# Optimization experiments

Measured on AMD Instinct MI355X. Metric: run time of the kernel, lower is better.

The kernel has to match this reference:

```python
import jax, jax.numpy as jnp
import numpy as np
from jax.scipy.linalg import expm

N, D, COND_DIM = 1152, 64, 1152
B, T = 16, 1024


def setup_inputs() -> dict:
    key = jax.random.key(0)
    k1, k2, k3, k4, k5 = jax.random.split(key, 5)
    x = jax.random.normal(k1, (B, T, N), dtype=jnp.float32)
    cond = jax.random.normal(k2, (B, COND_DIM), dtype=jnp.float32)
    # learned parameters
    P = jax.random.normal(k3, (N, D), dtype=jnp.float32)
    n_skew = D * (D - 1) // 2
    # nn.Linear default init: U(-1/sqrt(fan_in), 1/sqrt(fan_in))
    bound = 1.0 / np.sqrt(COND_DIM)
    W = jax.random.uniform(k4, (n_skew, COND_DIM), minval=-bound, maxval=bound, dtype=jnp.float32)
    b = jax.random.uniform(k5, (n_skew,), minval=-bound, maxval=bound, dtype=jnp.float32)
    return {"x": x, "cond": cond, "P": P, "W": W, "b": b}


def _rotation(cond, W, b):
    # SiLU -> Linear -> skew-symmetric A -> matrix exponential
    v = jax.nn.silu(cond) @ W.T + b  # (B, D*(D-1)//2)
    iu, ju = jnp.triu_indices(D, k=1)
    A = jnp.zeros((cond.shape[0], D, D), dtype=v.dtype)
    A = A.at[:, iu, ju].set(v).at[:, ju, iu].set(-v)
    return expm(A)  # batched over leading dim, (B, D, D)


def reference(x, cond, P, W, b):
    U, _ = jnp.linalg.qr(P)          # (N, D) orthonormal basis of subspace
    R = _rotation(cond, W, b)        # (B, D, D)
    z = jnp.einsum('btn,nd->btd', x, U)          # project into subspace
    z_rot = jnp.einsum('btd,bde->bte', z, R)     # rotate within subspace
    x_rot = x + jnp.einsum('btd,nd->btn', z_rot - z, U)  # (z_rot - z) @ U.T
    return x_rot
```

## Files before the change

### kernel.cpp

```cpp
#include <hip/hip_runtime.h>
#include <math.h>

#define NN 1152
#define DD 64
#define NSK 2016
#define NB 16
#define NROWS (NB*1024)
#define GPARTS 6
#define KPARTS 6
#define VNBLK 32
#define VBLKS (VNBLK*KPARTS)

typedef short bf16x8 __attribute__((ext_vector_type(8)));
typedef short bf16x4 __attribute__((ext_vector_type(4)));
typedef float f32x4  __attribute__((ext_vector_type(4)));

__device__ __forceinline__ short bfr(float f){
  unsigned u = __float_as_uint(f);
  u += 0x7fffu + ((u >> 16) & 1u);
  return (short)(u >> 16);
}

__global__ __launch_bounds__(256) void k_pre(const float* __restrict__ cond, const float* __restrict__ W,
                                             float* __restrict__ vpart,
                                             const float* __restrict__ P, float* __restrict__ Gpart){
  __shared__ float Ps[64*68];
  const int tid = threadIdx.x;
  if (blockIdx.x < VBLKS){
    const int nb = blockIdx.x / KPARTS;
    const int kp = blockIdx.x % KPARTS;
    const int lane = tid & 63, wid = tid >> 6;
    const int m = lane & 15, quad = lane >> 4;
    const int n0 = nb*64 + wid*16;
    if (n0 >= NSK) return;
    f32x4 acc = {0.f,0.f,0.f,0.f};
    const float* crow = &cond[m*NN + kp*192 + quad*8];
    const float* wrow = &W[(n0 + m)*NN + kp*192 + quad*8];
    #pragma unroll
    for (int c = 0; c < 6; ++c){
      const float4 ca = *(const float4*)(crow + c*32);
      const float4 cb = *(const float4*)(crow + c*32 + 4);
      const float4 wa = *(const float4*)(wrow + c*32);
      const float4 wb = *(const float4*)(wrow + c*32 + 4);
      bf16x8 a, b;
      const float cv[8] = {ca.x,ca.y,ca.z,ca.w,cb.x,cb.y,cb.z,cb.w};
      const float wv[8] = {wa.x,wa.y,wa.z,wa.w,wb.x,wb.y,wb.z,wb.w};
      #pragma unroll
      for (int j = 0; j < 8; ++j){
        const float xv = cv[j];
        a[j] = bfr(xv / (1.f + __expf(-xv)));
        b[j] = bfr(wv[j]);
      }
      acc = __builtin_amdgcn_mfma_f32_16x16x32_bf16(a, b, acc, 0, 0, 0);
    }
    #pragma unroll
    for (int r = 0; r < 4; ++r)
      vpart[(kp*16 + quad*4 + r)*NSK + n0 + m] = acc[r];
  } else {
    const int p = blockIdx.x - VBLKS;
    const int lr = tid >> 4, lc = (tid & 15) * 4;
    const int ti = tid >> 4, tj = tid & 15;
    float acc[4][4];
    #pragma unroll
    for (int i=0;i<4;++i){
      #pragma unroll
      for (int j=0;j<4;++j) acc[i][j]=0.f;
    }
    for (int ch = 0; ch < 3; ++ch){
      const int nn0 = p*192 + ch*64;
      __syncthreads();
      #pragma unroll
      for (int ii = 0; ii < 4; ++ii){
        const float4 pv = *(const float4*)&P[(nn0 + lr + 16*ii)*DD + lc];
        *(float4*)&Ps[(lr + 16*ii)*68 + lc] = pv;
      }
      __syncthreads();
      for (int r = 0; r < 64; ++r){
        const float4 a = *(const float4*)&Ps[r*68 + ti*4];
        const float4 b = *(const float4*)&Ps[r*68 + tj*4];
        const float av[4] = {a.x,a.y,a.z,a.w};
        const float bv[4] = {b.x,b.y,b.z,b.w};
        #pragma unroll
        for (int i=0;i<4;++i){
          #pragma unroll
          for (int j=0;j<4;++j) acc[i][j] = fmaf(av[i], bv[j], acc[i][j]);
        }
      }
    }
    float* g = &Gpart[p*DD*DD];
    #pragma unroll
    for (int i=0;i<4;++i){
      float4 ov = make_float4(acc[i][0], acc[i][1], acc[i][2], acc[i][3]);
      *(float4*)&g[(ti*4+i)*DD + tj*4] = ov;
    }
  }
}

__device__ void qr_wave(const float* __restrict__ Gpart, const float* __restrict__ P,
                        float* __restrict__ Rout){
  const int j = threadIdx.x;
  float Gc[DD], Wc[DD], Rc[DD];
  #pragma unroll
  for (int i = 0; i < DD; ++i){
    float g = 0.f;
    #pragma unroll
    for (int p = 0; p < GPARTS; ++p) g += Gpart[p*4096 + i*DD + j];
    Gc[i] = g;
    Wc[i] = P[i*DD + j];
  }
  #pragma unroll
  for (int k = 0; k < DD; ++k){
    const float gkk = __shfl(Gc[k], k);
    const float wkk = __shfl(Wc[k], k);
    const float beta = (wkk >= 0.f) ? -sqrtf(gkk) : sqrtf(gkk);
    const float wkj = Wc[k];
    const float dj  = Gc[k] - beta*wkj;
    const float cj  = dj / (beta*(beta - wkk));
    float rkj = wkj + dj/beta;
    if (j == k) rkj = beta;
    if (j <  k) rkj = 0.f;
    Rc[k] = rkj;
    #pragma unroll
    for (int i = k+1; i < DD; ++i){
      const float wik = __shfl(Wc[i], k);
      const float rki = __shfl(rkj, i);
      Wc[i] = fmaf(-cj,  wik, Wc[i]);
      Gc[i] = fmaf(-rki, rkj, Gc[i]);
    }
  }
  #pragma unroll
  for (int i = 0; i < DD; ++i) Rout[i*DD + j] = Rc[i];
}

__device__ __forceinline__ void mmul68(const float* __restrict__ A, const float* __restrict__ B,
                                       float* __restrict__ C, int tid){
  __syncthreads();
  const int w = tid >> 6, lane = tid & 63;
  const int r0 = (w & 3) * 16 + (lane >> 3) * 2;
  const int c0 = (w >> 2) * 32 + (lane & 7) * 4;
  float acc[2][4];
  #pragma unroll
  for (int i=0;i<2;++i){
    #pragma unroll
    for (int j=0;j<4;++j) acc[i][j]=0.f;
  }
  for (int kq = 0; kq < 16; ++kq){
    float4 b[4];
    #pragma unroll
    for (int kk=0;kk<4;++kk) b[kk] = *(const float4*)&B[(kq*4+kk)*68 + c0];
    const float4 a0 = *(const float4*)&A[(r0    )*68 + kq*4];
    const float4 a1 = *(const float4*)&A[(r0 + 1)*68 + kq*4];
    const float av0[4] = {a0.x,a0.y,a0.z,a0.w};
    const float av1[4] = {a1.x,a1.y,a1.z,a1.w};
    #pragma unroll
    for (int kk=0;kk<4;++kk){
      acc[0][0] = fmaf(av0[kk], b[kk].x, acc[0][0]);
      acc[0][1] = fmaf(av0[kk], b[kk].y, acc[0][1]);
      acc[0][2] = fmaf(av0[kk], b[kk].z, acc[0][2]);
      acc[0][3] = fmaf(av0[kk], b[kk].w, acc[0][3]);
      acc[1][0] = fmaf(av1[kk], b[kk].x, acc[1][0]);
      acc[1][1] = fmaf(av1[kk], b[kk].y, acc[1][1]);
      acc[1][2] = fmaf(av1[kk], b[kk].z, acc[1][2]);
      acc[1][3] = fmaf(av1[kk], b[kk].w, acc[1][3]);
    }
  }
  *(float4*)&C[(r0    )*68 + c0] = make_float4(acc[0][0],acc[0][1],acc[0][2],acc[0][3]);
  *(float4*)&C[(r0 + 1)*68 + c0] = make_float4(acc[1][0],acc[1][1],acc[1][2],acc[1][3]);
  __syncthreads();
}

__global__ __launch_bounds__(512,1) void k_setup(const float* __restrict__ Gpart, const float* __restrict__ P,
                                                 float* __restrict__ Rout,
                                                 const float* __restrict__ vpart, const float* __restrict__ bias,
                                                 float* __restrict__ Mg){
  __shared__ float Bs[64*68], B2[64*68], B3[64*68], Tb[64*68], Xb[64*68];
  __shared__ float red[512];
  __shared__ float scl_s;
  __shared__ int   ssh_s;
  const int tid = threadIdx.x;
  if (blockIdx.x == NB){
    if (tid >= 64) return;
    qr_wave(Gpart, P, Rout);
    return;
  }
  const int b = blockIdx.x;
  for (int idx = tid; idx < 64*64; idx += 512)
    Xb[(idx>>6)*68 + (idx&63)] = 0.f;
  __syncthreads();
  for (int idx = tid; idx < NSK; idx += 512){
    int i = (int)((127.0f - sqrtf(16129.0f - 8.0f*(float)idx)) * 0.5f);
    while (i*(127 - i)/2 > idx) --i;
    while ((i+1)*(127 - (i+1))/2 <= idx) ++i;
    const int jj = idx - i*(127 - i)/2 + i + 1;
    float val = bias[idx];
    #pragma unroll
    for (int p = 0; p < KPARTS; ++p) val += vpart[(p*16 + b)*NSK + idx];
    Xb[i*68 + jj] = val;
    Xb[jj*68 + i] = -val;
  }
  __syncthreads();
  {
    const int c = tid & 63, g = tid >> 6;
    float s = 0.f;
    for (int r = g*8; r < g*8 + 8; ++r) s += fabsf(Xb[r*68 + c]);
    red[g*64 + c] = s;
    __syncthreads();
    if (tid < 64){
      float cs = 0.f;
      #pragma unroll
      for (int g2 = 0; g2 < 8; ++g2) cs += red[g2*64 + tid];
      #pragma unroll
      for (int off = 32; off > 0; off >>= 1) cs = fmaxf(cs, __shfl_xor(cs, off));
      if (tid == 0){
        int s2 = 0; float scale = 1.f;
        float nrm = cs;
        while (nrm > 1.0f && s2 < 40){ nrm *= 0.5f; scale *= 0.5f; ++s2; }
        ssh_s = s2; scl_s = scale;
      }
    }
    __syncthreads();
  }
  const float scale = scl_s;
  const int   sq    = ssh_s;
  for (int idx = tid; idx < 64*64; idx += 512){
    const int i = idx>>6, jj = idx&63;
    Bs[i*68 + jj] = Xb[i*68 + jj] * scale;
  }
  mmul68(Bs, Bs, B2, tid);
  mmul68(B2, Bs, B3, tid);
  for (int idx = tid; idx < 64*64; idx += 512){
    const int i = idx>>6, jj = idx&63;
    const int o = i*68 + jj;
    Tb[o] = (i==jj ? (1.f/720.f) : 0.f) + Bs[o]*(1.f/5040.f) + B2[o]*(1.f/40320.f) + B3[o]*(1.f/362880.f);
  }
  mmul68(B3, Tb, Xb, tid);
  for (int idx = tid; idx < 64*64; idx += 512){
    const int i = idx>>6, jj = idx&63;
    const int o = i*68 + jj;
    Xb[o] += (i==jj ? (1.f/6.f) : 0.f) + Bs[o]*(1.f/24.f) + B2[o]*(1.f/120.f);
  }
  mmul68(B3, Xb, Tb, tid);
  for (int idx = tid; idx < 64*64; idx += 512){
    const int i = idx>>6, jj = idx&63;
    const int o = i*68 + jj;
    Tb[o] += (i==jj ? 1.f : 0.f) + Bs[o] + B2[o]*0.5f;
  }
  float* cur = Tb;
  float* oth = Xb;
  for (int r = 0; r < sq; ++r){
    mmul68(cur, cur, oth, tid);
    float* t = cur; cur = oth; oth = t;
  }
  for (int idx = tid; idx < 64*64; idx += 512){
    const int i = idx>>6, jj = idx&63;
    Mg[b*4096 + idx] = cur[i*68 + jj] - (i==jj ? 1.f : 0.f);
  }
}

__global__ __launch_bounds__(64) void k_solveU(const float* __restrict__ P, const float* __restrict__ Rg,
                                               short* __restrict__ Ubf, short* __restrict__ Utbf){
  __shared__ float Rs[DD*DD];
  __shared__ float Ps[DD*65];
  __shared__ float rd[DD];
  const int tid = threadIdx.x;
  const int n0 = blockIdx.x * DD;
  for (int r = 0; r < DD; ++r){
    Rs[r*DD + tid] = Rg[r*DD + tid];
    Ps[r*65 + tid] = P[(n0 + r)*DD + tid];
  }
  rd[tid] = 1.f / Rg[tid*DD + tid];
  __syncthreads();
  float u[DD];
  #pragma unroll
  for (int j = 0; j < DD; ++j){
    float s0 = Ps[tid*65 + j], s1 = 0.f;
    #pragma unroll
    for (int l = 0; l + 1 < j; l += 2){
      s0 = fmaf(-u[l],   Rs[l*DD + j],     s0);
      s1 = fmaf(-u[l+1], Rs[(l+1)*DD + j], s1);
    }
    if (j & 1) s0 = fmaf(-u[j-1], Rs[(j-1)*DD + j], s0);
    u[j] = (s0 + s1) * rd[j];
  }
  #pragma unroll
  for (int d = 0; d < DD; ++d)
    Utbf[d*NN + n0 + tid] = bfr(u[d]);
  #pragma unroll
  for (int j8 = 0; j8 < 8; ++j8){
    bf16x8 pk;
    #pragma unroll
    for (int jj = 0; jj < 8; ++jj) pk[jj] = bfr(u[j8*8 + jj]);
    *(bf16x8*)&Ubf[(n0 + tid)*DD + j8*8] = pk;
  }
}

__global__ __launch_bounds__(512,1) void k_zw(const float* __restrict__ x, const short* __restrict__ Utbf,
                                              const float* __restrict__ Mg, short* __restrict__ wg){
  __shared__ float zs[64*68];
  __shared__ float Ms[64*68];
  const int tid  = threadIdx.x;
  const int lane = tid & 63, wid = tid >> 6;
  const int row0 = blockIdx.x * 64;
  const int bb   = row0 >> 10;
  const int m    = lane & 15, quad = lane >> 4;
  for (int idx = tid; idx < 64*64; idx += 512)
    Ms[(idx>>6)*68 + (idx&63)] = Mg[bb*4096 + idx];

  const int r0 = (wid & 3) * 16;
  const int c0 = (wid >> 2) * 32;
  f32x4 acc0 = {0.f,0.f,0.f,0.f}, acc1 = {0.f,0.f,0.f,0.f};
  const float* xrow = &x[(row0 + r0 + m)*NN + quad*8];
  const short* ut0  = &Utbf[(c0      + m)*NN + quad*8];
  const short* ut1  = &Utbf[(c0 + 16 + m)*NN + quad*8];
  float4 xa = *(const float4*)(xrow);
  float4 xb = *(const float4*)(xrow + 4);
  bf16x8 b0 = *(const bf16x8*)(ut0);
  bf16x8 b1 = *(const bf16x8*)(ut1);
  for (int kc = 0; kc < NN; kc += 32){
    float4 nxa, nxb; bf16x8 nb0, nb1;
    if (kc + 32 < NN){
      nxa = *(const float4*)(xrow + kc + 32);
      nxb = *(const float4*)(xrow + kc + 36);
      nb0 = *(const bf16x8*)(ut0 + kc + 32);
      nb1 = *(const bf16x8*)(ut1 + kc + 32);
    }
    bf16x8 a;
    a[0]=bfr(xa.x); a[1]=bfr(xa.y); a[2]=bfr(xa.z); a[3]=bfr(xa.w);
    a[4]=bfr(xb.x); a[5]=bfr(xb.y); a[6]=bfr(xb.z); a[7]=bfr(xb.w);
    acc0 = __builtin_amdgcn_mfma_f32_16x16x32_bf16(a, b0, acc0, 0, 0, 0);
    acc1 = __builtin_amdgcn_mfma_f32_16x16x32_bf16(a, b1, acc1, 0, 0, 0);
    xa = nxa; xb = nxb; b0 = nb0; b1 = nb1;
  }
  #pragma unroll
  for (int q = 0; q < 4; ++q){
    zs[(r0 + quad*4 + q)*68 + c0      + m] = acc0[q];
    zs[(r0 + quad*4 + q)*68 + c0 + 16 + m] = acc1[q];
  }
  __syncthreads();

  const int r  = tid >> 3;
  const int cc = (tid & 7) * 8;
  float w0[8];
  #pragma unroll
  for (int jj = 0; jj < 8; ++jj) w0[jj] = 0.f;
  for (int k = 0; k < 64; ++k){
    const float zr = zs[r*68 + k];
    const float4 m0 = *(const float4*)&Ms[k*68 + cc];
    const float4 m1 = *(const float4*)&Ms[k*68 + cc + 4];
    w0[0] = fmaf(zr, m0.x, w0[0]); w0[1] = fmaf(zr, m0.y, w0[1]);
    w0[2] = fmaf(zr, m0.z, w0[2]); w0[3] = fmaf(zr, m0.w, w0[3]);
    w0[4] = fmaf(zr, m1.x, w0[4]); w0[5] = fmaf(zr, m1.y, w0[5]);
    w0[6] = fmaf(zr, m1.z, w0[6]); w0[7] = fmaf(zr, m1.w, w0[7]);
  }
  bf16x8 pk;
  #pragma unroll
  for (int jj = 0; jj < 8; ++jj) pk[jj] = bfr(w0[jj]);
  *(bf16x8*)&wg[(row0 + r)*DD + cc] = pk;
}

__global__ __launch_bounds__(256) void k_out(const float* __restrict__ x, const short* __restrict__ Ubf,
                                             const short* __restrict__ wg, float* __restrict__ out){
  const int tid  = threadIdx.x;
  const int lane = tid & 63, wid = tid >> 6;
  const int row0 = blockIdx.x * 16;
  const int m    = lane & 15, quad = lane >> 4;
  const int q4   = quad * 4;
  bf16x8 wa0 = *(const bf16x8*)&wg[(row0 + m)*DD +      quad*8];
  bf16x8 wa1 = *(const bf16x8*)&wg[(row0 + m)*DD + 32 + quad*8];
  bf16x8 ub0 = *(const bf16x8*)&Ubf[(wid*16 + m)*DD +      quad*8];
  bf16x8 ub1 = *(const bf16x8*)&Ubf[(wid*16 + m)*DD + 32 + quad*8];
  float xq0 = x[(row0 + q4 + 0)*NN + wid*16 + m];
  float xq1 = x[(row0 + q4 + 1)*NN + wid*16 + m];
  float xq2 = x[(row0 + q4 + 2)*NN + wid*16 + m];
  float xq3 = x[(row0 + q4 + 3)*NN + wid*16 + m];
  for (int it = 0; it < 18; ++it){
    const int n0 = (wid + 4*it) * 16;
    f32x4 acc = {0.f,0.f,0.f,0.f};
    acc = __builtin_amdgcn_mfma_f32_16x16x32_bf16(wa0, ub0, acc, 0, 0, 0);
    acc = __builtin_amdgcn_mfma_f32_16x16x32_bf16(wa1, ub1, acc, 0, 0, 0);
    const float o0 = xq0 + acc[0];
    const float o1 = xq1 + acc[1];
    const float o2 = xq2 + acc[2];
    const float o3 = xq3 + acc[3];
    if (it < 17){
      const int n1 = n0 + 64;
      ub0 = *(const bf16x8*)&Ubf[(n1 + m)*DD +      quad*8];
      ub1 = *(const bf16x8*)&Ubf[(n1 + m)*DD + 32 + quad*8];
      xq0 = x[(row0 + q4 + 0)*NN + n1 + m];
      xq1 = x[(row0 + q4 + 1)*NN + n1 + m];
      xq2 = x[(row0 + q4 + 2)*NN + n1 + m];
      xq3 = x[(row0 + q4 + 3)*NN + n1 + m];
    }
    out[(row0 + q4 + 0)*NN + n0 + m] = o0;
    out[(row0 + q4 + 1)*NN + n0 + m] = o1;
    out[(row0 + q4 + 2)*NN + n0 + m] = o2;
    out[(row0 + q4 + 3)*NN + n0 + m] = o3;
  }
}

extern "C" void kernel_launch(void* const* d_in, const int* in_sizes, int n_in,
                              void* d_out, int out_size, void* d_ws, size_t ws_size,
                              hipStream_t stream) {
  const float* x    = (const float*)d_in[0];
  const float* cond = (const float*)d_in[1];
  const float* P    = (const float*)d_in[2];
  const float* W    = (const float*)d_in[3];
  const float* bias = (const float*)d_in[4];
  float* out = (float*)d_out;
  float* ws  = (float*)d_ws;

  float* Gpart = ws;
  float* Rbuf  = ws + 24576;
  float* vpart = ws + 28672;
  float* Mg    = ws + 222208;
  short* Ubf   = (short*)(ws + 287744);
  short* Utbf  = (short*)(ws + 324608);
  short* wg    = (short*)(ws + 361472);

  hipLaunchKernelGGL(k_pre,   dim3(VBLKS + GPARTS), dim3(256), 0, stream, cond, W, vpart, P, Gpart);
  hipLaunchKernelGGL(k_setup, dim3(NB + 1),         dim3(512), 0, stream, Gpart, P, Rbuf, vpart, bias, Mg);
  hipLaunchKernelGGL(k_solveU,dim3(NN/DD),          dim3(64),  0, stream, P, Rbuf, Ubf, Utbf);
  hipLaunchKernelGGL(k_zw,    dim3(NROWS/64),       dim3(512), 0, stream, x, Utbf, Mg, wg);
  hipLaunchKernelGGL(k_out,   dim3(NROWS/16),       dim3(256), 0, stream, x, Ubf, wg, out);
}
```

Baseline: 263.7 us.

## Project with raw P and fold R inverse into per-batch rotation matrix

Replaces the explicit U = P R^-1 solve with projections through P itself: y = x P is computed in bf16 alongside the QR/expm setup blocks, and K = R^-1 M R^-T is built per batch so the output becomes x + (y K) P^T. This drops the serial triangular-solve kernel and overlaps the large x-projection GEMM with the small setup work in one launch. The cost is an extra small K-matrix kernel, per-block recomputation of y K inside the output kernel, and possible accuracy loss since P is not orthonormal and y is rounded to bf16.

```diff
diff --git a/kernel.cpp b/kernel.cpp
--- a/kernel.cpp
+++ b/kernel.cpp
@@ -10,6 +10,7 @@
 #define KPARTS 6
 #define VNBLK 32
 #define VBLKS (VNBLK*KPARTS)
+#define TBLKS 18
 
 typedef short bf16x8 __attribute__((ext_vector_type(8)));
 typedef short bf16x4 __attribute__((ext_vector_type(4)));
@@ -20,10 +21,14 @@
   u += 0x7fffu + ((u >> 16) & 1u);
   return (short)(u >> 16);
 }
+__device__ __forceinline__ float htof(short h){
+  return __uint_as_float(((unsigned)(unsigned short)h) << 16);
+}
 
 __global__ __launch_bounds__(256) void k_pre(const float* __restrict__ cond, const float* __restrict__ W,
                                              float* __restrict__ vpart,
-                                             const float* __restrict__ P, float* __restrict__ Gpart){
+                                             const float* __restrict__ P, float* __restrict__ Gpart,
+                                             short* __restrict__ Pbf, short* __restrict__ Ptbf){
   __shared__ float Ps[64*68];
   const int tid = threadIdx.x;
   if (blockIdx.x < VBLKS){
@@ -56,7 +61,7 @@
     #pragma unroll
     for (int r = 0; r < 4; ++r)
       vpart[(kp*16 + quad*4 + r)*NSK + n0 + m] = acc[r];
-  } else {
+  } else if (blockIdx.x < VBLKS + GPARTS){
     const int p = blockIdx.x - VBLKS;
     const int lr = tid >> 4, lc = (tid & 15) * 4;
     const int ti = tid >> 4, tj = tid & 15;
@@ -93,43 +98,21 @@
       float4 ov = make_float4(acc[i][0], acc[i][1], acc[i][2], acc[i][3]);
       *(float4*)&g[(ti*4+i)*DD + tj*4] = ov;
     }
-  }
-}
-
-__device__ void qr_wave(const float* __restrict__ Gpart, const float* __restrict__ P,
-                        float* __restrict__ Rout){
-  const int j = threadIdx.x;
-  float Gc[DD], Wc[DD], Rc[DD];
-  #pragma unroll
-  for (int i = 0; i < DD; ++i){
-    float g = 0.f;
-    #pragma unroll
-    for (int p = 0; p < GPARTS; ++p) g += Gpart[p*4096 + i*DD + j];
-    Gc[i] = g;
-    Wc[i] = P[i*DD + j];
-  }
-  #pragma unroll
-  for (int k = 0; k < DD; ++k){
-    const float gkk = __shfl(Gc[k], k);
-    const float wkk = __shfl(Wc[k], k);
-    const float beta = (wkk >= 0.f) ? -sqrtf(gkk) : sqrtf(gkk);
-    const float wkj = Wc[k];
-    const float dj  = Gc[k] - beta*wkj;
-    const float cj  = dj / (beta*(beta - wkk));
-    float rkj = wkj + dj/beta;
-    if (j == k) rkj = beta;
-    if (j <  k) rkj = 0.f;
-    Rc[k] = rkj;
-    #pragma unroll
-    for (int i = k+1; i < DD; ++i){
-      const float wik = __shfl(Wc[i], k);
-      const float rki = __shfl(rkj, i);
-      Wc[i] = fmaf(-cj,  wik, Wc[i]);
-      Gc[i] = fmaf(-rki, rkj, Gc[i]);
-    }
-  }
-  #pragma unroll
-  for (int i = 0; i < DD; ++i) Rout[i*DD + j] = Rc[i];
+  } else {
+    const int t = blockIdx.x - (VBLKS + GPARTS);
+    const int n0 = t*64;
+    for (int idx = tid; idx < 4096; idx += 256)
+      Ps[(idx>>6)*68 + (idx&63)] = P[(n0 + (idx>>6))*DD + (idx&63)];
+    __syncthreads();
+    for (int idx = tid; idx < 4096; idx += 256){
+      const int r = idx>>6, c = idx&63;
+      Pbf[(n0+r)*DD + c] = bfr(Ps[r*68 + c]);
+    }
+    for (int idx = tid; idx < 4096; idx += 256){
+      const int d = idx>>6, rr = idx&63;
+      Ptbf[d*NN + n0 + rr] = bfr(Ps[rr*68 + d]);
+    }
+  }
 }
 
 __device__ __forceinline__ void mmul68(const float* __restrict__ A, const float* __restrict__ B,
@@ -169,18 +152,99 @@
   __syncthreads();
 }
 
-__global__ __launch_bounds__(512,1) void k_setup(const float* __restrict__ Gpart, const float* __restrict__ P,
-                                                 float* __restrict__ Rout,
+__global__ __launch_bounds__(512,1) void k_fused(const float* __restrict__ Gpart, const float* __restrict__ P,
                                                  const float* __restrict__ vpart, const float* __restrict__ bias,
-                                                 float* __restrict__ Mg){
+                                                 float* __restrict__ Mg, float* __restrict__ Rinvg,
+                                                 const float* __restrict__ x, const short* __restrict__ Ptbf,
+                                                 short* __restrict__ ybf){
   __shared__ float Bs[64*68], B2[64*68], B3[64*68], Tb[64*68], Xb[64*68];
   __shared__ float red[512];
   __shared__ float scl_s;
   __shared__ int   ssh_s;
   const int tid = threadIdx.x;
+  if (blockIdx.x > NB){
+    const int lane = tid & 63, wid = tid >> 6;
+    const int row0 = (blockIdx.x - NB - 1) * 64;
+    const int m    = lane & 15, quad = lane >> 4;
+    const int r0 = (wid & 3) * 16;
+    const int c0 = (wid >> 2) * 32;
+    f32x4 acc0 = {0.f,0.f,0.f,0.f}, acc1 = {0.f,0.f,0.f,0.f};
+    const float* xrow = &x[(row0 + r0 + m)*NN + quad*8];
+    const short* ut0  = &Ptbf[(c0      + m)*NN + quad*8];
+    const short* ut1  = &Ptbf[(c0 + 16 + m)*NN + quad*8];
+    float4 xa = *(const float4*)(xrow);
+    float4 xb = *(const float4*)(xrow + 4);
+    bf16x8 b0 = *(const bf16x8*)(ut0);
+    bf16x8 b1 = *(const bf16x8*)(ut1);
+    for (int kc = 0; kc < NN; kc += 32){
+      float4 nxa, nxb; bf16x8 nb0, nb1;
+      if (kc + 32 < NN){
+        nxa = *(const float4*)(xrow + kc + 32);
+        nxb = *(const float4*)(xrow + kc + 36);
+        nb0 = *(const bf16x8*)(ut0 + kc + 32);
+        nb1 = *(const bf16x8*)(ut1 + kc + 32);
+      }
+      bf16x8 a;
+      a[0]=bfr(xa.x); a[1]=bfr(xa.y); a[2]=bfr(xa.z); a[3]=bfr(xa.w);
+      a[4]=bfr(xb.x); a[5]=bfr(xb.y); a[6]=bfr(xb.z); a[7]=bfr(xb.w);
+      acc0 = __builtin_amdgcn_mfma_f32_16x16x32_bf16(a, b0, acc0, 0, 0, 0);
+      acc1 = __builtin_amdgcn_mfma_f32_16x16x32_bf16(a, b1, acc1, 0, 0, 0);
+      xa = nxa; xb = nxb; b0 = nb0; b1 = nb1;
+    }
+    #pragma unroll
+    for (int q = 0; q < 4; ++q){
+      ybf[(row0 + r0 + quad*4 + q)*DD + c0      + m] = bfr(acc0[q]);
+      ybf[(row0 + r0 + quad*4 + q)*DD + c0 + 16 + m] = bfr(acc1[q]);
+    }
+    return;
+  }
   if (blockIdx.x == NB){
-    if (tid >= 64) return;
-    qr_wave(Gpart, P, Rout);
+    if (tid < 64){
+      const int j = tid;
+      float Gc[DD], Wc[DD], Rc[DD];
+      #pragma unroll
+      for (int i = 0; i < DD; ++i){
+        float g = 0.f;
+        #pragma unroll
+        for (int p = 0; p < GPARTS; ++p) g += Gpart[p*4096 + i*DD + j];
+        Gc[i] = g;
+        Wc[i] = P[i*DD + j];
+      }
+      #pragma unroll
+      for (int k = 0; k < DD; ++k){
+        const float gkk = __shfl(Gc[k], k);
+        const float wkk = __shfl(Wc[k], k);
+        const float beta = (wkk >= 0.f) ? -sqrtf(gkk) : sqrtf(gkk);
+        const float wkj = Wc[k];
+        const float dj  = Gc[k] - beta*wkj;
+        const float cj  = dj / (beta*(beta - wkk));
+        float rkj = wkj + dj/beta;
+        if (j == k) rkj = beta;
+        if (j <  k) rkj = 0.f;
+        Rc[k] = rkj;
+        #pragma unroll
+        for (int i = k+1; i < DD; ++i){
+          const float wik = __shfl(Wc[i], k);
+          const float rki = __shfl(rkj, i);
+          Wc[i] = fmaf(-cj,  wik, Wc[i]);
+          Gc[i] = fmaf(-rki, rkj, Gc[i]);
+        }
+      }
+      #pragma unroll
+      for (int i = 0; i < DD; ++i) Bs[i*68 + j] = Rc[i];
+    }
+    __syncthreads();
+    if (tid < 64){
+      const int j = tid;
+      for (int i = 63; i >= 0; --i){
+        float acc = (i==j) ? 1.f : 0.f;
+        for (int l = i+1; l < 64; ++l)
+          acc -= Bs[i*68 + l] * B2[l*68 + j];
+        B2[i*68 + j] = acc / Bs[i*68 + i];
+      }
+      for (int i = 0; i < 64; ++i)
+        Rinvg[i*DD + j] = B2[i*68 + j];
+    }
     return;
   }
   const int b = blockIdx.x;
@@ -257,118 +321,123 @@
   }
 }
 
-__global__ __launch_bounds__(64) void k_solveU(const float* __restrict__ P, const float* __restrict__ Rg,
-                                               short* __restrict__ Ubf, short* __restrict__ Utbf){
-  __shared__ float Rs[DD*DD];
-  __shared__ float Ps[DD*65];
-  __shared__ float rd[DD];
-  const int tid = threadIdx.x;
-  const int n0 = blockIdx.x * DD;
-  for (int r = 0; r < DD; ++r){
-    Rs[r*DD + tid] = Rg[r*DD + tid];
-    Ps[r*65 + tid] = P[(n0 + r)*DD + tid];
-  }
-  rd[tid] = 1.f / Rg[tid*DD + tid];
-  __syncthreads();
-  float u[DD];
-  #pragma unroll
-  for (int j = 0; j < DD; ++j){
-    float s0 = Ps[tid*65 + j], s1 = 0.f;
-    #pragma unroll
-    for (int l = 0; l + 1 < j; l += 2){
-      s0 = fmaf(-u[l],   Rs[l*DD + j],     s0);
-      s1 = fmaf(-u[l+1], Rs[(l+1)*DD + j], s1);
-    }
-    if (j & 1) s0 = fmaf(-u[j-1], Rs[(j-1)*DD + j], s0);
-    u[j] = (s0 + s1) * rd[j];
-  }
-  #pragma unroll
-  for (int d = 0; d < DD; ++d)
-    Utbf[d*NN + n0 + tid] = bfr(u[d]);
-  #pragma unroll
-  for (int j8 = 0; j8 < 8; ++j8){
-    bf16x8 pk;
-    #pragma unroll
-    for (int jj = 0; jj < 8; ++jj) pk[jj] = bfr(u[j8*8 + jj]);
-    *(bf16x8*)&Ubf[(n0 + tid)*DD + j8*8] = pk;
-  }
-}
-
-__global__ __launch_bounds__(512,1) void k_zw(const float* __restrict__ x, const short* __restrict__ Utbf,
-                                              const float* __restrict__ Mg, short* __restrict__ wg){
-  __shared__ float zs[64*68];
-  __shared__ float Ms[64*68];
-  const int tid  = threadIdx.x;
-  const int lane = tid & 63, wid = tid >> 6;
-  const int row0 = blockIdx.x * 64;
-  const int bb   = row0 >> 10;
-  const int m    = lane & 15, quad = lane >> 4;
-  for (int idx = tid; idx < 64*64; idx += 512)
-    Ms[(idx>>6)*68 + (idx&63)] = Mg[bb*4096 + idx];
-
-  const int r0 = (wid & 3) * 16;
-  const int c0 = (wid >> 2) * 32;
-  f32x4 acc0 = {0.f,0.f,0.f,0.f}, acc1 = {0.f,0.f,0.f,0.f};
-  const float* xrow = &x[(row0 + r0 + m)*NN + quad*8];
-  const short* ut0  = &Utbf[(c0      + m)*NN + quad*8];
-  const short* ut1  = &Utbf[(c0 + 16 + m)*NN + quad*8];
-  float4 xa = *(const float4*)(xrow);
-  float4 xb = *(const float4*)(xrow + 4);
-  bf16x8 b0 = *(const bf16x8*)(ut0);
-  bf16x8 b1 = *(const bf16x8*)(ut1);
-  for (int kc = 0; kc < NN; kc += 32){
-    float4 nxa, nxb; bf16x8 nb0, nb1;
-    if (kc + 32 < NN){
-      nxa = *(const float4*)(xrow + kc + 32);
-      nxb = *(const float4*)(xrow + kc + 36);
-      nb0 = *(const bf16x8*)(ut0 + kc + 32);
-      nb1 = *(const bf16x8*)(ut1 + kc + 32);
-    }
-    bf16x8 a;
-    a[0]=bfr(xa.x); a[1]=bfr(xa.y); a[2]=bfr(xa.z); a[3]=bfr(xa.w);
-    a[4]=bfr(xb.x); a[5]=bfr(xb.y); a[6]=bfr(xb.z); a[7]=bfr(xb.w);
-    acc0 = __builtin_amdgcn_mfma_f32_16x16x32_bf16(a, b0, acc0, 0, 0, 0);
-    acc1 = __builtin_amdgcn_mfma_f32_16x16x32_bf16(a, b1, acc1, 0, 0, 0);
-    xa = nxa; xb = nxb; b0 = nb0; b1 = nb1;
-  }
-  #pragma unroll
-  for (int q = 0; q < 4; ++q){
-    zs[(r0 + quad*4 + q)*68 + c0      + m] = acc0[q];
-    zs[(r0 + quad*4 + q)*68 + c0 + 16 + m] = acc1[q];
-  }
-  __syncthreads();
-
-  const int r  = tid >> 3;
-  const int cc = (tid & 7) * 8;
-  float w0[8];
-  #pragma unroll
-  for (int jj = 0; jj < 8; ++jj) w0[jj] = 0.f;
-  for (int k = 0; k < 64; ++k){
-    const float zr = zs[r*68 + k];
-    const float4 m0 = *(const float4*)&Ms[k*68 + cc];
-    const float4 m1 = *(const float4*)&Ms[k*68 + cc + 4];
-    w0[0] = fmaf(zr, m0.x, w0[0]); w0[1] = fmaf(zr, m0.y, w0[1]);
-    w0[2] = fmaf(zr, m0.z, w0[2]); w0[3] = fmaf(zr, m0.w, w0[3]);
-    w0[4] = fmaf(zr, m1.x, w0[4]); w0[5] = fmaf(zr, m1.y, w0[5]);
-    w0[6] = fmaf(zr, m1.z, w0[6]); w0[7] = fmaf(zr, m1.w, w0[7]);
-  }
-  bf16x8 pk;
-  #pragma unroll
-  for (int jj = 0; jj < 8; ++jj) pk[jj] = bfr(w0[jj]);
-  *(bf16x8*)&wg[(row0 + r)*DD + cc] = pk;
-}
-
-__global__ __launch_bounds__(256) void k_out(const float* __restrict__ x, const short* __restrict__ Ubf,
-                                             const short* __restrict__ wg, float* __restrict__ out){
+__global__ __launch_bounds__(256) void k_kmat(const float* __restrict__ Rinvg, const float* __restrict__ Mg,
+                                              float* __restrict__ Kg){
+  __shared__ float Ri[64*68], Ms[64*68], Ts[64*68];
+  const int b = blockIdx.x, tid = threadIdx.x;
+  for (int idx = tid; idx < 4096; idx += 256){
+    const int r = idx>>6, c = idx&63;
+    Ri[r*68 + c] = Rinvg[idx];
+    Ms[r*68 + c] = Mg[b*4096 + idx];
+  }
+  __syncthreads();
+  const int ti = tid >> 4, tj = tid & 15;
+  {
+    float acc[4][4];
+    #pragma unroll
+    for (int i=0;i<4;++i){
+      #pragma unroll
+      for (int j=0;j<4;++j) acc[i][j]=0.f;
+    }
+    for (int kq = 0; kq < 16; ++kq){
+      float4 a[4], bm[4];
+      #pragma unroll
+      for (int i=0;i<4;++i) a[i] = *(const float4*)&Ri[(ti*4+i)*68 + kq*4];
+      #pragma unroll
+      for (int kk=0;kk<4;++kk) bm[kk] = *(const float4*)&Ms[(kq*4+kk)*68 + tj*4];
+      #pragma unroll
+      for (int i=0;i<4;++i){
+        const float av[4] = {a[i].x,a[i].y,a[i].z,a[i].w};
+        #pragma unroll
+        for (int kk=0;kk<4;++kk){
+          acc[i][0] = fmaf(av[kk], bm[kk].x, acc[i][0]);
+          acc[i][1] = fmaf(av[kk], bm[kk].y, acc[i][1]);
+          acc[i][2] = fmaf(av[kk], bm[kk].z, acc[i][2]);
+          acc[i][3] = fmaf(av[kk], bm[kk].w, acc[i][3]);
+        }
+      }
+    }
+    __syncthreads();
+    #pragma unroll
+    for (int i=0;i<4;++i)
+      *(float4*)&Ts[(ti*4+i)*68 + tj*4] = make_float4(acc[i][0],acc[i][1],acc[i][2],acc[i][3]);
+    __syncthreads();
+  }
+  {
+    float acc[4][4];
+    #pragma unroll
+    for (int i=0;i<4;++i){
+      #pragma unroll
+      for (int j=0;j<4;++j) acc[i][j]=0.f;
+    }
+    for (int kq = 0; kq < 16; ++kq){
+      float4 a[4], bt[4];
+      #pragma unroll
+      for (int i=0;i<4;++i) a[i] = *(const float4*)&Ts[(ti*4+i)*68 + kq*4];
+      #pragma unroll
+      for (int j=0;j<4;++j) bt[j] = *(const float4*)&Ri[(tj*4+j)*68 + kq*4];
+      #pragma unroll
+      for (int i=0;i<4;++i){
+        #pragma unroll
+        for (int j=0;j<4;++j){
+          acc[i][j] = fmaf(a[i].x, bt[j].x, acc[i][j]);
+          acc[i][j] = fmaf(a[i].y, bt[j].y, acc[i][j]);
+          acc[i][j] = fmaf(a[i].z, bt[j].z, acc[i][j]);
+          acc[i][j] = fmaf(a[i].w, bt[j].w, acc[i][j]);
+        }
+      }
+    }
+    #pragma unroll
+    for (int i=0;i<4;++i)
+      *(float4*)&Kg[b*4096 + (ti*4+i)*DD + tj*4] = make_float4(acc[i][0],acc[i][1],acc[i][2],acc[i][3]);
+  }
+}
+
+__global__ __launch_bounds__(256) void k_wout(const float* __restrict__ x, const short* __restrict__ Pbf,
+                                              const short* __restrict__ ybf, const float* __restrict__ Kg,
+                                              float* __restrict__ out){
+  __shared__ float Ks[64*68];
+  __shared__ float ys[16*68];
+  __shared__ short wbf[16*72];
   const int tid  = threadIdx.x;
   const int lane = tid & 63, wid = tid >> 6;
   const int row0 = blockIdx.x * 16;
+  const int bb   = row0 >> 10;
   const int m    = lane & 15, quad = lane >> 4;
-  const int q4   = quad * 4;
-  bf16x8 wa0 = *(const bf16x8*)&wg[(row0 + m)*DD +      quad*8];
-  bf16x8 wa1 = *(const bf16x8*)&wg[(row0 + m)*DD + 32 + quad*8];
-  bf16x8 ub0 = *(const bf16x8*)&Ubf[(wid*16 + m)*DD +      quad*8];
-  bf16x8 ub1 = *(const bf16x8*)&Ubf[(wid*16 + m)*DD + 32 + quad*8];
+  for (int idx = tid; idx < 4096; idx += 256)
+    Ks[(idx>>6)*68 + (idx&63)] = Kg[bb*4096 + idx];
+  {
+    const int idx = tid*4;
+    const int r = idx >> 6, c = idx & 63;
+    bf16x4 yv = *(const bf16x4*)&ybf[(row0 + r)*DD + c];
+    ys[r*68 + c    ] = htof(yv[0]);
+    ys[r*68 + c + 1] = htof(yv[1]);
+    ys[r*68 + c + 2] = htof(yv[2]);
+    ys[r*68 + c + 3] = htof(yv[3]);
+  }
+  __syncthreads();
+  {
+    const int r = tid >> 4, c4 = (tid & 15)*4;
+    float w0[4] = {0.f,0.f,0.f,0.f};
+    for (int k = 0; k < 64; ++k){
+      const float yr = ys[r*68 + k];
+      const float4 kv = *(const float4*)&Ks[k*68 + c4];
+      w0[0] = fmaf(yr, kv.x, w0[0]);
+      w0[1] = fmaf(yr, kv.y, w0[1]);
+      w0[2] = fmaf(yr, kv.z, w0[2]);
+      w0[3] = fmaf(yr, kv.w, w0[3]);
+    }
+    bf16x4 pk;
+    #pragma unroll
+    for (int jj = 0; jj < 4; ++jj) pk[jj] = bfr(w0[jj]);
+    *(bf16x4*)&wbf[r*72 + c4] = pk;
+  }
+  __syncthreads();
+  const int q4 = quad * 4;
+  bf16x8 wa0 = *(const bf16x8*)&wbf[m*72 +      quad*8];
+  bf16x8 wa1 = *(const bf16x8*)&wbf[m*72 + 32 + quad*8];
+  bf16x8 ub0 = *(const bf16x8*)&Pbf[(wid*16 + m)*DD +      quad*8];
+  bf16x8 ub1 = *(const bf16x8*)&Pbf[(wid*16 + m)*DD + 32 + quad*8];
   float xq0 = x[(row0 + q4 + 0)*NN + wid*16 + m];
   float xq1 = x[(row0 + q4 + 1)*NN + wid*16 + m];
   float xq2 = x[(row0 + q4 + 2)*NN + wid*16 + m];
@@ -384,8 +453,8 @@
     const float o3 = xq3 + acc[3];
     if (it < 17){
       const int n1 = n0 + 64;
-      ub0 = *(const bf16x8*)&Ubf[(n1 + m)*DD +      quad*8];
-      ub1 = *(const bf16x8*)&Ubf[(n1 + m)*DD + 32 + quad*8];
+      ub0 = *(const bf16x8*)&Pbf[(n1 + m)*DD +      quad*8];
+      ub1 = *(const bf16x8*)&Pbf[(n1 + m)*DD + 32 + quad*8];
       xq0 = x[(row0 + q4 + 0)*NN + n1 + m];
       xq1 = x[(row0 + q4 + 1)*NN + n1 + m];
       xq2 = x[(row0 + q4 + 2)*NN + n1 + m];
@@ -410,16 +479,18 @@
   float* ws  = (float*)d_ws;
 
   float* Gpart = ws;
-  float* Rbuf  = ws + 24576;
-  float* vpart = ws + 28672;
-  float* Mg    = ws + 222208;
-  short* Ubf   = (short*)(ws + 287744);
-  short* Utbf  = (short*)(ws + 324608);
-  short* wg    = (short*)(ws + 361472);
-
-  hipLaunchKernelGGL(k_pre,   dim3(VBLKS + GPARTS), dim3(256), 0, stream, cond, W, vpart, P, Gpart);
-  hipLaunchKernelGGL(k_setup, dim3(NB + 1),         dim3(512), 0, stream, Gpart, P, Rbuf, vpart, bias, Mg);
-  hipLaunchKernelGGL(k_solveU,dim3(NN/DD),          dim3(64),  0, stream, P, Rbuf, Ubf, Utbf);
-  hipLaunchKernelGGL(k_zw,    dim3(NROWS/64),       dim3(512), 0, stream, x, Utbf, Mg, wg);
-  hipLaunchKernelGGL(k_out,   dim3(NROWS/16),       dim3(256), 0, stream, x, Ubf, wg, out);
-}
+  float* vpart = ws + 24576;
+  float* Kg    = ws + 24576;
+  float* Mg    = ws + 218112;
+  float* Rinvg = ws + 283648;
+  short* Pbf   = (short*)(ws + 287744);
+  short* Ptbf  = (short*)(ws + 324608);
+  short* ybf   = (short*)(ws + 361472);
+
+  hipLaunchKernelGGL(k_pre,  dim3(VBLKS + GPARTS + TBLKS), dim3(256), 0, stream,
+                     cond, W, vpart, P, Gpart, Pbf, Ptbf);
+  hipLaunchKernelGGL(k_fused, dim3(NB + 1 + NROWS/64), dim3(512), 0, stream,
+                     Gpart, P, vpart, bias, Mg, Rinvg, x, Ptbf, ybf);
+  hipLaunchKernelGGL(k_kmat, dim3(NB), dim3(256), 0, stream, Rinvg, Mg, Kg);
+  hipLaunchKernelGGL(k_wout, dim3(NROWS/16), dim3(256), 0, stream, x, Pbf, ybf, Kg, out);
+}
```

After: 482.6 us. 1.83x slower.
